# Kernel tuning notes

Measured on AMD Instinct MI355X. Metric: run time of the kernel, lower is better.

The kernel has to match this reference:

```python
import jax, jax.numpy as jnp
import numpy as np

N_HEADS, INPUT_DIM, EMBED_DIM = 8, 128, 128
KEY_DIM = EMBED_DIM // N_HEADS  # val_dim = key_dim = 16
B, N = 8, 1024


def setup_inputs() -> dict:
    key = jax.random.key(0)
    ks = jax.random.split(key, 16)
    stdv_k = 1.0 / np.sqrt(KEY_DIM)
    stdv_e = 1.0 / np.sqrt(EMBED_DIM)

    def U(k, shape, s):
        return jax.random.uniform(k, shape, jnp.float32, -s, s)

    hdk = (N_HEADS, INPUT_DIM, KEY_DIM)
    hke = (N_HEADS, KEY_DIM, EMBED_DIM)
    return {
        "q_n": jax.random.normal(ks[0], (B, N, INPUT_DIM), jnp.float32),
        "q_c": jax.random.normal(ks[1], (B, N, INPUT_DIM), jnp.float32),
        "mask": jax.random.bernoulli(ks[2], 0.5, (B, N, N)),
        "W_query_n": U(ks[3], hdk, stdv_k),
        "W_key_nn": U(ks[4], hdk, stdv_k),
        "W_val_nn": U(ks[5], hdk, stdv_k),
        "W_key_c": U(ks[6], hdk, stdv_k),
        "W_val_c": U(ks[7], hdk, stdv_k),
        "W_query_c": U(ks[8], hdk, stdv_k),
        "W_key_n": U(ks[9], hdk, stdv_k),
        "W_val_n": U(ks[10], hdk, stdv_k),
        "W_out_node": U(ks[11], hke, stdv_e),
        "W_out_color": U(ks[12], hke, stdv_e),
    }


def reference(q_n, q_c, mask, W_query_n, W_key_nn, W_val_nn, W_key_c, W_val_c,
              W_query_c, W_key_n, W_val_n, W_out_node, W_out_color):
    norm = 1.0 / jnp.sqrt(jnp.asarray(KEY_DIM, q_n.dtype))
    neg_inf = jnp.asarray(-jnp.inf, q_n.dtype)

    def proj(x, W):  # (B,N,D), (H,D,K) -> (H,B,N,K)
        return jnp.einsum('bnd,hdk->hbnk', x, W)

    # --- color stream: q_c attends over nodes q_n ---
    Q_c = proj(q_c, W_query_c)
    K_n = proj(q_n, W_key_n)
    V_n = proj(q_n, W_val_n)
    attn_c = jax.nn.softmax(norm * jnp.einsum('hbqk,hbnk->hbqn', Q_c, K_n), axis=-1)
    heads_c = jnp.einsum('hbqn,hbnv->hbqv', attn_c, V_n)
    out_color = jnp.einsum('hbqv,hve->bqe', heads_c, W_out_color)

    # --- node stream: masked self-attention + attention over colors ---
    Q_n = proj(q_n, W_query_n)
    K_nn = proj(q_n, W_key_nn)
    V_nn = proj(q_n, W_val_nn)
    comp_nn = norm * jnp.einsum('hbqk,hbnk->hbqn', Q_n, K_nn)
    m = mask[None]  # (1,B,Q,N) broadcast over heads; True = not allowed
    comp_nn = jnp.where(m, neg_inf, comp_nn)
    attn_nn = jax.nn.softmax(comp_nn, axis=-1)
    attn_nn = jnp.where(m, jnp.asarray(0.0, q_n.dtype), attn_nn)
    heads_nn = jnp.einsum('hbqn,hbnv->hbqv', attn_nn, V_nn)

    K_nc = proj(q_c, W_key_c)
    V_nc = proj(q_c, W_val_c)
    attn_nc = jax.nn.softmax(norm * jnp.einsum('hbqk,hbnk->hbqn', Q_n, K_nc), axis=-1)
    heads_nc = jnp.einsum('hbqn,hbnv->hbqv', attn_nc, V_nc)

    heads = heads_nn + heads_nc
    out = jnp.einsum('hbqv,hve->bqe', heads, W_out_node)
    return (out, out_color)
```

## Files before the change

kernel.cpp:

```cpp
#include <hip/hip_runtime.h>
#include <stdint.h>

#define NH 8
#define NB 8
#define NN 1024
#define ND 128
#define NK 16
#define NF (NB*NN)
#define C2EXP 0.36067376022224085f
#define LSTR 136

typedef float f32x16 __attribute__((ext_vector_type(16)));
typedef short bf16x8 __attribute__((ext_vector_type(8)));

__device__ __forceinline__ uint16_t f2bf(float f){
  uint32_t x = __float_as_uint(f);
  uint32_t r = (x + 0x7fffu + ((x>>16)&1u)) >> 16;
  return (uint16_t)r;
}
__device__ __forceinline__ float fast_exp2(float x){
#if __has_builtin(__builtin_amdgcn_exp2f)
  return __builtin_amdgcn_exp2f(x);
#else
  return exp2f(x);
#endif
}

__global__ __launch_bounds__(256) void pack_kernel(const int* __restrict__ mask,
                                                   uint32_t* __restrict__ packN){
  const int w = threadIdx.x >> 6, lane = threadIdx.x & 63;
  const int row = blockIdx.x*4 + w;
  const int* mp = mask + (size_t)row*NN;
  uint32_t* dst = packN + (size_t)row*32;
  for (int wq = 0; wq < 16; ++wq) {
    int v = mp[wq*64 + lane];
    unsigned long long bal = __ballot(v != 0);
    if (lane == 0) { dst[wq*2] = (uint32_t)bal; dst[wq*2+1] = (uint32_t)(bal>>32); }
  }
}

struct ProjArgs { const float* x[8]; const float* w[8]; };

__global__ __launch_bounds__(256) void proj_kernel(ProjArgs args, uint16_t* ws){
  __shared__ __align__(16) uint16_t WT[128*LSTR];
  __shared__ __align__(16) uint16_t S[128*LSTR];
  const int p = blockIdx.y;
  const int rb = blockIdx.x;
  const int tid = threadIdx.x;

  const float4* w4 = (const float4*)args.w[p];
  #pragma unroll
  for (int i = 0; i < 16; ++i) {
    int e4 = i*256 + tid;
    float4 f = w4[e4];
    int e = e4*4;
    int h = e >> 11, d = (e >> 4) & 127, k = e & 15;
    uint16_t* wr = &WT[(h*16 + k)*LSTR + d];
    wr[0*LSTR] = f2bf(f.x); wr[1*LSTR] = f2bf(f.y);
    wr[2*LSTR] = f2bf(f.z); wr[3*LSTR] = f2bf(f.w);
  }
  __syncthreads();

  const int wave = tid >> 6, lane = tid & 63;
  const int l5 = lane >> 5, lm = lane & 31;
  const int r0 = rb*128 + wave*32;
  const float* xrow = args.x[p] + (size_t)(r0 + lm)*ND + l5*8;

  bf16x8 afr[8];
  #pragma unroll
  for (int kt = 0; kt < 8; ++kt) {
    float4 f0 = *(const float4*)(xrow + kt*16);
    float4 f1 = *(const float4*)(xrow + kt*16 + 4);
    bf16x8 a;
    a[0]=f2bf(f0.x); a[1]=f2bf(f0.y); a[2]=f2bf(f0.z); a[3]=f2bf(f0.w);
    a[4]=f2bf(f1.x); a[5]=f2bf(f1.y); a[6]=f2bf(f1.z); a[7]=f2bf(f1.w);
    afr[kt] = a;
  }

  const bool tr = (p==2)|(p==5)|(p==7);
  const float qsc = (p==0 || p==3) ? C2EXP : 1.0f;
  #pragma unroll
  for (int nt = 0; nt < 4; ++nt) {
    f32x16 acc;
    #pragma unroll
    for (int i = 0; i < 16; ++i) acc[i] = 0.f;
    #pragma unroll
    for (int kt = 0; kt < 8; ++kt) {
      bf16x8 b = *(const bf16x8*)(&WT[(nt*32 + lm)*LSTR + kt*16 + l5*8]);
      acc = __builtin_amdgcn_mfma_f32_32x32x16_bf16(afr[kt], b, acc, 0, 0, 0);
    }
    #pragma unroll
    for (int i = 0; i < 16; ++i) {
      int r = wave*32 + (i&3) + 8*(i>>2) + 4*l5;
      int c = nt*32 + lm;
      if (tr) {
        int t2 = (r>>2)&3;
        int rp = (t2==1 || t2==2) ? (r^12) : r;
        S[c*LSTR + rp] = f2bf(acc[i]);
      } else {
        S[r*LSTR + c] = f2bf(acc[i]*qsc);
      }
    }
  }
  __syncthreads();

  uint16_t* dst = ws + (size_t)p*((size_t)NH*NF*NK);
  if (!tr) {
    #pragma unroll
    for (int it = 0; it < 8; ++it) {
      int c = it*256 + tid;
      int row = c >> 4, cg = c & 15;
      bf16x8 v = *(const bf16x8*)(&S[row*LSTR + cg*8]);
      int h = cg >> 1, k8 = cg & 1;
      *(bf16x8*)(dst + ((size_t)h*NF + rb*128 + row)*NK + k8*8) = v;
    }
  } else {
    const int b = rb >> 3, nb = (rb & 7)*128;
    #pragma unroll
    for (int it = 0; it < 8; ++it) {
      int c = it*256 + tid;
      int col = c >> 4, ng = c & 15;
      bf16x8 v = *(const bf16x8*)(&S[col*LSTR + ng*8]);
      int h = col >> 4, k = col & 15;
      *(bf16x8*)(dst + ((size_t)(h*NB + b)*NK + k)*NN + nb + ng*8) = v;
    }
  }
}

template<bool MASKED>
__device__ __forceinline__ void attn_stream(
    const uint4* __restrict__ kbuf, bf16x8 aq,
    const uint16_t* __restrict__ VTb, const uint4* __restrict__ pmw4,
    int nh, int l5, int lm, f32x16& O)
{
  f32x16 Z;
  #pragma unroll
  for (int i = 0; i < 16; ++i) Z[i] = 0.f;
  for (int t4 = 0; t4 < 4; ++t4) {
    uint4 mq;
    if (MASKED) mq = pmw4[nh*4 + t4];
    #pragma unroll
    for (int j = 0; j < 4; ++j) {
      const int n0 = (nh*16 + t4*4 + j)*32;
      bf16x8 bk = *(const bf16x8*)(&kbuf[l5*1024 + n0 + lm]);
      f32x16 St = __builtin_amdgcn_mfma_f32_32x32x16_bf16(bk, aq, Z, 0, 0, 0);
      uint32_t mws = 0;
      if (MASKED) {
        uint32_t mw = (j==0) ? mq.x : (j==1) ? mq.y : (j==2) ? mq.z : mq.w;
        mws = mw >> (4*l5);
      }
      float p[16];
      #pragma unroll
      for (int i = 0; i < 16; ++i) {
        float pv = fast_exp2(St[i]);
        if (MASKED && ((mws >> ((i&3) + 8*(i>>2))) & 1u)) pv = 0.f;
        p[i] = pv;
      }
      union { uint32_t u[4]; bf16x8 v; } B1, B2;
      #pragma unroll
      for (int k = 0; k < 4; ++k) {
        B1.u[k] = __builtin_amdgcn_perm(__float_as_uint(p[2*k+1]),
                                        __float_as_uint(p[2*k]),   0x07060302u);
        B2.u[k] = __builtin_amdgcn_perm(__float_as_uint(p[2*k+9]),
                                        __float_as_uint(p[2*k+8]), 0x07060302u);
      }
      bf16x8 av1, av2;
      #pragma unroll
      for (int i = 0; i < 8; ++i) { av1[i] = 0; av2[i] = 0; }
      if (lm < 16) {
        const uint16_t* vp = VTb + (size_t)lm*NN + n0 + l5*8;
        av1 = *(const bf16x8*)(vp);
        av2 = *(const bf16x8*)(vp + 16);
      } else if (lm == 16) {
        #pragma unroll
        for (int i = 0; i < 8; ++i) { av1[i] = (short)0x3F80; av2[i] = (short)0x3F80; }
      }
      O = __builtin_amdgcn_mfma_f32_32x32x16_bf16(av1, B1.v, O, 0, 0, 0);
      O = __builtin_amdgcn_mfma_f32_32x32x16_bf16(av2, B2.v, O, 0, 0, 0);
    }
  }
}

__global__ __launch_bounds__(512, 4) void attn_kernel(
    const uint16_t* __restrict__ Qn_, const uint16_t* __restrict__ K1n,
    const uint16_t* __restrict__ V1n, const uint16_t* __restrict__ K2n,
    const uint16_t* __restrict__ V2n,
    const uint16_t* __restrict__ Qc_, const uint16_t* __restrict__ K1c,
    const uint16_t* __restrict__ V1c,
    const uint32_t* __restrict__ packN,
    uint16_t* __restrict__ hn_, uint16_t* __restrict__ hc_)
{
  __shared__ uint4 kbuf[2048];
  const bool dual = (blockIdx.z == 0);
  const uint16_t* Q   = dual ? Qn_ : Qc_;
  const uint16_t* K1  = dual ? K1n : K1c;
  uint16_t* outp      = dual ? hn_ : hc_;

  const int hb = blockIdx.y;
  const int h = hb >> 3, b = hb & 7;
  const size_t base = ((size_t)h*NF + (size_t)b*NN)*NK;
  const int tid = threadIdx.x;

  const uint4* k1 = (const uint4*)(K1 + base);
  for (int i = tid; i < 2048; i += 512)
    kbuf[(i & 1)*1024 + (i >> 1)] = k1[i];
  __syncthreads();

  const int wave = tid >> 6, lane = tid & 63;
  const int l5 = lane >> 5, lm = lane & 31;
  const int qt = wave & 3, nh = wave >> 2;
  const int q = blockIdx.x*128 + qt*32 + lm;

  const bf16x8 aq = *(const bf16x8*)(Q + base + (size_t)q*NK + l5*8);
  const uint4* pmw4 = (const uint4*)(packN + ((size_t)b*NN + q)*32);

  f32x16 O1, O2;
  #pragma unroll
  for (int i = 0; i < 16; ++i) { O1[i] = 0.f; O2[i] = 0.f; }

  if (dual) {
    attn_stream<true>(kbuf, aq, V1n + (size_t)hb*(NK*NN), pmw4, nh, l5, lm, O1);
    __syncthreads();
    const uint4* k2 = (const uint4*)(K2n + base);
    for (int i = tid; i < 2048; i += 512)
      kbuf[(i & 1)*1024 + (i >> 1)] = k2[i];
    __syncthreads();
    attn_stream<false>(kbuf, aq, V2n + (size_t)hb*(NK*NN), nullptr, nh, l5, lm, O2);
  } else {
    attn_stream<false>(kbuf, aq, V1c + (size_t)hb*(NK*NN), nullptr, nh, l5, lm, O1);
  }

  float L1 = O1[8] + __shfl_xor(O1[8], 32, 64);
  float L2 = O2[8] + __shfl_xor(O2[8], 32, 64);

  __syncthreads();
  float* cw = ((float*)kbuf) + ((size_t)(qt*2 + l5)*32 + lm)*18;
  if (nh == 1) {
    #pragma unroll
    for (int i = 0; i < 8; ++i) cw[i] = O1[i];
    if (dual) {
      #pragma unroll
      for (int i = 0; i < 8; ++i) cw[8+i] = O2[i];
    }
    cw[16] = L1; cw[17] = L2;
  }
  __syncthreads();
  if (nh == 0) {
    const float l1 = L1 + cw[16];
    const float i1 = (l1 > 0.f) ? 1.f/l1 : 0.f;
    float i2 = 0.f;
    if (dual) { const float l2 = L2 + cw[17]; i2 = (l2 > 0.f) ? 1.f/l2 : 0.f; }
    uint32_t w[4];
    #pragma unroll
    for (int k = 0; k < 4; ++k) {
      float va = (O1[2*k]   + cw[2*k])  *i1;
      float vb = (O1[2*k+1] + cw[2*k+1])*i1;
      if (dual) { va += (O2[2*k] + cw[8+2*k])*i2; vb += (O2[2*k+1] + cw[8+2*k+1])*i2; }
      w[k] = ((uint32_t)f2bf(vb) << 16) | f2bf(va);
    }
    uint16_t* hp = outp + ((size_t)b*NN + q)*128 + h*16 + l5*4;
    *(uint2*)(hp)     = make_uint2(w[0], w[1]);
    *(uint2*)(hp + 8) = make_uint2(w[2], w[3]);
  }
}

__global__ __launch_bounds__(256) void outproj_kernel(
    const uint16_t* __restrict__ hn, const uint16_t* __restrict__ hc,
    const float* __restrict__ wn, const float* __restrict__ wc,
    float* __restrict__ out)
{
  __shared__ __align__(16) uint16_t WT[128*LSTR];
  const int s = blockIdx.y;
  const int rb = blockIdx.x;
  const int tid = threadIdx.x;
  const float* wsrc = s ? wc : wn;
  const float4* w4 = (const float4*)wsrc;
  #pragma unroll
  for (int i = 0; i < 16; ++i) {
    int e4 = i*256 + tid;
    float4 f = w4[e4];
    int e = e4*4;
    int c = e >> 7, col = e & 127;
    uint16_t* wr = &WT[col*LSTR + c];
    wr[0*LSTR] = f2bf(f.x); wr[1*LSTR] = f2bf(f.y);
    wr[2*LSTR] = f2bf(f.z); wr[3*LSTR] = f2bf(f.w);
  }
  __syncthreads();

  const int wave = tid >> 6, lane = tid & 63;
  const int l5 = lane >> 5, lm = lane & 31;
  const int rt = wave & 1, nh2 = wave >> 1;
  const int r0 = rb*64 + rt*32;
  const uint16_t* hp = (s ? hc : hn) + (size_t)(r0 + lm)*128 + l5*8;
  bf16x8 afr[8];
  #pragma unroll
  for (int kt = 0; kt < 8; ++kt) afr[kt] = *(const bf16x8*)(hp + kt*16);

  float* dst = out + (size_t)s*((size_t)NF*ND) + (size_t)r0*ND;
  #pragma unroll
  for (int nt2 = 0; nt2 < 2; ++nt2) {
    const int nt = nh2*2 + nt2;
    f32x16 acc;
    #pragma unroll
    for (int i = 0; i < 16; ++i) acc[i] = 0.f;
    #pragma unroll
    for (int kt = 0; kt < 8; ++kt) {
      bf16x8 b = *(const bf16x8*)(&WT[(nt*32 + lm)*LSTR + kt*16 + l5*8]);
      acc = __builtin_amdgcn_mfma_f32_32x32x16_bf16(afr[kt], b, acc, 0, 0, 0);
    }
    #pragma unroll
    for (int i = 0; i < 16; ++i) {
      int r = (i&3) + 8*(i>>2) + 4*l5;
      dst[(size_t)r*ND + nt*32 + lm] = acc[i];
    }
  }
}

extern "C" void kernel_launch(void* const* d_in, const int* in_sizes, int n_in,
                              void* d_out, int out_size, void* d_ws, size_t ws_size,
                              hipStream_t stream)
{
  const float* q_n = (const float*)d_in[0];
  const float* q_c = (const float*)d_in[1];
  const int* mask = (const int*)d_in[2];
  const float* W[10];
  for (int i = 0; i < 10; ++i) W[i] = (const float*)d_in[3+i];

  uint16_t* ws16 = (uint16_t*)d_ws;
  const size_t PE = (size_t)NH*NF*NK;
  uint16_t* Qc   = ws16 + 0*PE;
  uint16_t* Kn   = ws16 + 1*PE;
  uint16_t* VTn  = ws16 + 2*PE;
  uint16_t* Qn   = ws16 + 3*PE;
  uint16_t* Knn  = ws16 + 4*PE;
  uint16_t* VTnn = ws16 + 5*PE;
  uint16_t* Knc  = ws16 + 6*PE;
  uint16_t* VTnc = ws16 + 7*PE;
  uint16_t* heads_node = ws16 + 8*PE;
  uint32_t* packN   = (uint32_t*)(ws16 + 9*PE);
  uint16_t* heads_c = ws16 + 10*PE;

  pack_kernel<<<2048, 256, 0, stream>>>(mask, packN);

  ProjArgs pa;
  pa.x[0]=q_c; pa.w[0]=W[5];
  pa.x[1]=q_n; pa.w[1]=W[6];
  pa.x[2]=q_n; pa.w[2]=W[7];
  pa.x[3]=q_n; pa.w[3]=W[0];
  pa.x[4]=q_n; pa.w[4]=W[1];
  pa.x[5]=q_n; pa.w[5]=W[2];
  pa.x[6]=q_c; pa.w[6]=W[3];
  pa.x[7]=q_c; pa.w[7]=W[4];
  proj_kernel<<<dim3(64, 8), 256, 0, stream>>>(pa, ws16);

  attn_kernel<<<dim3(8, 64, 2), 512, 0, stream>>>(
      Qn, Knn, VTnn, Knc, VTnc, Qc, Kn, VTn, packN,
      heads_node, heads_c);

  outproj_kernel<<<dim3(128, 2), 256, 0, stream>>>(heads_node, heads_c,
                                                   W[8], W[9], (float*)d_out);
}
```

Measured before the change: 167.6 us.

## Software-pipeline attention loop: prefetch next V tile and QK MFMA

Flattens the 4x4 inner attention loop into a 16-step fully unrolled loop that issues the next tile's QK^T MFMA and V global loads before the current tile's exp/pack/PV work. It also preloads all mask words up front. The constant ones row used for the softmax denominator now comes from a ones buffer written by the pack kernel, so lanes lm<17 share one load path instead of branching. This aims to hide global load and MFMA latency, at the cost of more live registers, which could cut occupancy under launch_bounds(512,4).

```diff
diff --git a/kernel.cpp b/kernel.cpp
--- a/kernel.cpp
+++ b/kernel.cpp
@@ -27,7 +27,11 @@
 }
 
 __global__ __launch_bounds__(256) void pack_kernel(const int* __restrict__ mask,
-                                                   uint32_t* __restrict__ packN){
+                                                   uint32_t* __restrict__ packN,
+                                                   uint16_t* __restrict__ onesw){
+  if (blockIdx.x == 0) {
+    for (int i = threadIdx.x; i < 1024; i += 256) onesw[i] = 0x3F80;
+  }
   const int w = threadIdx.x >> 6, lane = threadIdx.x & 63;
   const int row = blockIdx.x*4 + w;
   const int* mp = mask + (size_t)row*NN;
@@ -130,54 +134,71 @@
 template<bool MASKED>
 __device__ __forceinline__ void attn_stream(
     const uint4* __restrict__ kbuf, bf16x8 aq,
-    const uint16_t* __restrict__ VTb, const uint4* __restrict__ pmw4,
+    const uint16_t* __restrict__ vbase, const uint4* __restrict__ pmw4,
     int nh, int l5, int lm, f32x16& O)
 {
   f32x16 Z;
   #pragma unroll
   for (int i = 0; i < 16; ++i) Z[i] = 0.f;
-  for (int t4 = 0; t4 < 4; ++t4) {
-    uint4 mq;
-    if (MASKED) mq = pmw4[nh*4 + t4];
-    #pragma unroll
-    for (int j = 0; j < 4; ++j) {
-      const int n0 = (nh*16 + t4*4 + j)*32;
-      bf16x8 bk = *(const bf16x8*)(&kbuf[l5*1024 + n0 + lm]);
-      f32x16 St = __builtin_amdgcn_mfma_f32_32x32x16_bf16(bk, aq, Z, 0, 0, 0);
-      uint32_t mws = 0;
-      if (MASKED) {
-        uint32_t mw = (j==0) ? mq.x : (j==1) ? mq.y : (j==2) ? mq.z : mq.w;
-        mws = mw >> (4*l5);
+
+  uint32_t mw[16];
+  if (MASKED) {
+    uint4 m0 = pmw4[nh*4+0], m1 = pmw4[nh*4+1];
+    uint4 m2 = pmw4[nh*4+2], m3 = pmw4[nh*4+3];
+    mw[0]=m0.x; mw[1]=m0.y; mw[2]=m0.z; mw[3]=m0.w;
+    mw[4]=m1.x; mw[5]=m1.y; mw[6]=m1.z; mw[7]=m1.w;
+    mw[8]=m2.x; mw[9]=m2.y; mw[10]=m2.z; mw[11]=m2.w;
+    mw[12]=m3.x; mw[13]=m3.y; mw[14]=m3.z; mw[15]=m3.w;
+  }
+
+  const int base_n = nh*512;
+  const bool vload = (lm < 17);
+
+  bf16x8 av1, av2, av1n, av2n;
+  #pragma unroll
+  for (int i = 0; i < 8; ++i) { av1[i]=0; av2[i]=0; av1n[i]=0; av2n[i]=0; }
+  if (vload) {
+    const uint16_t* vp = vbase + base_n + l5*8;
+    av1 = *(const bf16x8*)(vp);
+    av2 = *(const bf16x8*)(vp + 16);
+  }
+  f32x16 Stc = __builtin_amdgcn_mfma_f32_32x32x16_bf16(
+      *(const bf16x8*)(&kbuf[l5*1024 + base_n + lm]), aq, Z, 0, 0, 0);
+
+  #pragma unroll
+  for (int t = 0; t < 16; ++t) {
+    f32x16 Stn;
+    if (t < 15) {
+      const int n1 = base_n + (t+1)*32;
+      if (vload) {
+        const uint16_t* vp = vbase + n1 + l5*8;
+        av1n = *(const bf16x8*)(vp);
+        av2n = *(const bf16x8*)(vp + 16);
       }
-      float p[16];
-      #pragma unroll
-      for (int i = 0; i < 16; ++i) {
-        float pv = fast_exp2(St[i]);
-        if (MASKED && ((mws >> ((i&3) + 8*(i>>2))) & 1u)) pv = 0.f;
-        p[i] = pv;
-      }
-      union { uint32_t u[4]; bf16x8 v; } B1, B2;
-      #pragma unroll
-      for (int k = 0; k < 4; ++k) {
-        B1.u[k] = __builtin_amdgcn_perm(__float_as_uint(p[2*k+1]),
-                                        __float_as_uint(p[2*k]),   0x07060302u);
-        B2.u[k] = __builtin_amdgcn_perm(__float_as_uint(p[2*k+9]),
-                                        __float_as_uint(p[2*k+8]), 0x07060302u);
-      }
-      bf16x8 av1, av2;
-      #pragma unroll
-      for (int i = 0; i < 8; ++i) { av1[i] = 0; av2[i] = 0; }
-      if (lm < 16) {
-        const uint16_t* vp = VTb + (size_t)lm*NN + n0 + l5*8;
-        av1 = *(const bf16x8*)(vp);
-        av2 = *(const bf16x8*)(vp + 16);
-      } else if (lm == 16) {
-        #pragma unroll
-        for (int i = 0; i < 8; ++i) { av1[i] = (short)0x3F80; av2[i] = (short)0x3F80; }
-      }
-      O = __builtin_amdgcn_mfma_f32_32x32x16_bf16(av1, B1.v, O, 0, 0, 0);
-      O = __builtin_amdgcn_mfma_f32_32x32x16_bf16(av2, B2.v, O, 0, 0, 0);
-    }
+      Stn = __builtin_amdgcn_mfma_f32_32x32x16_bf16(
+          *(const bf16x8*)(&kbuf[l5*1024 + n1 + lm]), aq, Z, 0, 0, 0);
+    }
+
+    const uint32_t mws = MASKED ? (mw[t] >> (4*l5)) : 0u;
+    float p[16];
+    #pragma unroll
+    for (int i = 0; i < 16; ++i) {
+      float pv = fast_exp2(Stc[i]);
+      if (MASKED && ((mws >> ((i&3) + 8*(i>>2))) & 1u)) pv = 0.f;
+      p[i] = pv;
+    }
+    union { uint32_t u[4]; bf16x8 v; } B1, B2;
+    #pragma unroll
+    for (int k = 0; k < 4; ++k) {
+      B1.u[k] = __builtin_amdgcn_perm(__float_as_uint(p[2*k+1]),
+                                      __float_as_uint(p[2*k]),   0x07060302u);
+      B2.u[k] = __builtin_amdgcn_perm(__float_as_uint(p[2*k+9]),
+                                      __float_as_uint(p[2*k+8]), 0x07060302u);
+    }
+    O = __builtin_amdgcn_mfma_f32_32x32x16_bf16(av1, B1.v, O, 0, 0, 0);
+    O = __builtin_amdgcn_mfma_f32_32x32x16_bf16(av2, B2.v, O, 0, 0, 0);
+
+    if (t < 15) { Stc = Stn; av1 = av1n; av2 = av2n; }
   }
 }
 
@@ -187,7 +208,7 @@
     const uint16_t* __restrict__ V2n,
     const uint16_t* __restrict__ Qc_, const uint16_t* __restrict__ K1c,
     const uint16_t* __restrict__ V1c,
-    const uint32_t* __restrict__ packN,
+    const uint32_t* __restrict__ packN, const uint16_t* __restrict__ onesb,
     uint16_t* __restrict__ hn_, uint16_t* __restrict__ hc_)
 {
   __shared__ uint4 kbuf[2048];
@@ -214,20 +235,25 @@
   const bf16x8 aq = *(const bf16x8*)(Q + base + (size_t)q*NK + l5*8);
   const uint4* pmw4 = (const uint4*)(packN + ((size_t)b*NN + q)*32);
 
+  const uint16_t* VT1 = (dual ? V1n : V1c) + (size_t)hb*(NK*NN);
+  const uint16_t* vb1 = (lm < 16) ? (VT1 + (size_t)lm*NN) : onesb;
+
   f32x16 O1, O2;
   #pragma unroll
   for (int i = 0; i < 16; ++i) { O1[i] = 0.f; O2[i] = 0.f; }
 
   if (dual) {
-    attn_stream<true>(kbuf, aq, V1n + (size_t)hb*(NK*NN), pmw4, nh, l5, lm, O1);
+    attn_stream<true>(kbuf, aq, vb1, pmw4, nh, l5, lm, O1);
     __syncthreads();
     const uint4* k2 = (const uint4*)(K2n + base);
     for (int i = tid; i < 2048; i += 512)
       kbuf[(i & 1)*1024 + (i >> 1)] = k2[i];
     __syncthreads();
-    attn_stream<false>(kbuf, aq, V2n + (size_t)hb*(NK*NN), nullptr, nh, l5, lm, O2);
+    const uint16_t* VT2 = V2n + (size_t)hb*(NK*NN);
+    const uint16_t* vb2 = (lm < 16) ? (VT2 + (size_t)lm*NN) : onesb;
+    attn_stream<false>(kbuf, aq, vb2, nullptr, nh, l5, lm, O2);
   } else {
-    attn_stream<false>(kbuf, aq, V1c + (size_t)hb*(NK*NN), nullptr, nh, l5, lm, O1);
+    attn_stream<false>(kbuf, aq, vb1, nullptr, nh, l5, lm, O1);
   }
 
   float L1 = O1[8] + __shfl_xor(O1[8], 32, 64);
@@ -339,8 +365,9 @@
   uint16_t* heads_node = ws16 + 8*PE;
   uint32_t* packN   = (uint32_t*)(ws16 + 9*PE);
   uint16_t* heads_c = ws16 + 10*PE;
-
-  pack_kernel<<<2048, 256, 0, stream>>>(mask, packN);
+  uint16_t* onesb   = ws16 + 11*PE;
+
+  pack_kernel<<<2048, 256, 0, stream>>>(mask, packN, onesb);
 
   ProjArgs pa;
   pa.x[0]=q_c; pa.w[0]=W[5];
@@ -354,7 +381,7 @@
   proj_kernel<<<dim3(64, 8), 256, 0, stream>>>(pa, ws16);
 
   attn_kernel<<<dim3(8, 64, 2), 512, 0, stream>>>(
-      Qn, Knn, VTnn, Knc, VTnc, Qc, Kn, VTn, packN,
+      Qn, Knn, VTnn, Knc, VTnc, Qc, Kn, VTn, packN, onesb,
       heads_node, heads_c);
 
   outproj_kernel<<<dim3(128, 2), 256, 0, stream>>>(heads_node, heads_c,
```

After: 165.2 us. About the same (-1.4%).
